# Performance work log

Measured on AMD Instinct MI355X. Metric: run time of the kernel, lower is better.

Reference implementation:

```python
import jax, jax.numpy as jnp
import numpy as np

EPS = 1e-12  # matches torch F.normalize eps

def _l2_normalize(x):
    n = jnp.linalg.norm(x, axis=-1, keepdims=True)
    return x / jnp.maximum(n, EPS)

def setup_inputs() -> dict:
    key = jax.random.key(0)
    k1, k2, k3 = jax.random.split(key, 3)
    B, D, C = 2048, 1024, 65536
    return {
        "query": jax.random.normal(k1, (B, D), dtype=jnp.float32),
        "memory_keys": jax.random.normal(k2, (C, D), dtype=jnp.float32),
        "memory_values": jax.random.normal(k3, (C, D), dtype=jnp.float32),
        "memory_usage": jnp.zeros((C,), dtype=jnp.float32),
        "k": 8,
    }

def reference(query, memory_keys, memory_values, memory_usage, k):
    # cosine similarity: [B, C]
    qn = _l2_normalize(query)
    mn = _l2_normalize(memory_keys)
    sims = jnp.matmul(qn, mn.T)
    # top-k indices per query: [B, k]
    _, indices = jax.lax.top_k(sims, k)
    # gather retrieved keys/values: [B, k, D]
    retrieved_keys = memory_keys[indices]
    retrieved_values = memory_values[indices]
    # usage scatter-add (+1 per retrieved slot), vectorized form of the loop
    capacity = memory_usage.shape[0]
    counts = jax.ops.segment_sum(
        jnp.ones(indices.size, dtype=memory_usage.dtype),
        indices.reshape(-1),
        num_segments=capacity,
    )
    usage_new = memory_usage + counts
    return retrieved_keys, retrieved_values, usage_new
```

## Files before the change

kernel.cpp:

```cpp
#include <hip/hip_runtime.h>
#include <math.h>

#define BQ 2048
#define DD 1024
#define CC 65536
#define KSEL 8
#define NSTRIPE 32
#define SC (CC / NSTRIPE)
#define GTM 128
#define GTN 128
#define GBK 32
#define NTILES (SC / GTN)
#define LCAND 8
#define TRES 32

typedef unsigned int u32;
typedef unsigned short ushort_t;
typedef __attribute__((ext_vector_type(8))) short bf16x8;
typedef __attribute__((ext_vector_type(4))) float f32x4;


#define FENCE() asm volatile("" ::: "memory")
#define LGKM0() asm volatile("s_waitcnt lgkmcnt(0)" ::: "memory")

__device__ __forceinline__ ushort_t f2bf(float f) {
    u32 u = __builtin_bit_cast(u32, f);
    return (ushort_t)((u + 0x7FFFu + ((u >> 16) & 1u)) >> 16);
}

__device__ __forceinline__ void gl_lds16(const ushort_t* g, ushort_t* l) {
    __builtin_amdgcn_global_load_lds(
        (const __attribute__((address_space(1))) u32*)g,
        (__attribute__((address_space(3))) u32*)l, 16, 0, 0);
}

__global__ __launch_bounds__(256) void normconv_kernel(
    const float* __restrict__ q, const float* __restrict__ keys,
    double* __restrict__ qinv, double* __restrict__ kinv,
    ushort_t* __restrict__ qn, ushort_t* __restrict__ kn)
{
    __shared__ double red[4];
    const int row = blockIdx.x;
    const int t = threadIdx.x;
    const bool iskey = row < CC;
    const float* src = iskey ? keys + (size_t)row * DD
                             : q + (size_t)(row - CC) * DD;
    float4 v = ((const float4*)src)[t];
    double s = (double)v.x * v.x + (double)v.y * v.y +
               (double)v.z * v.z + (double)v.w * v.w;
    for (int off = 32; off > 0; off >>= 1) s += __shfl_down(s, off);
    if ((t & 63) == 0) red[t >> 6] = s;
    __syncthreads();
    const double tot = red[0] + red[1] + red[2] + red[3];
    const double inv = 1.0 / fmax(sqrt(tot), 1e-12);
    if (t == 0) {
        if (iskey) kinv[row] = inv; else qinv[row - CC] = inv;
    }
    const float invf = (float)inv;
    ushort4 o;
    o.x = f2bf(v.x * invf); o.y = f2bf(v.y * invf);
    o.z = f2bf(v.z * invf); o.w = f2bf(v.w * invf);
    ushort_t* dst = iskey ? kn + (size_t)row * DD
                          : qn + (size_t)(row - CC) * DD;
    ((ushort4*)dst)[t] = o;
}

__global__ __launch_bounds__(256, 2) void gemm_topk_kernel(
    const ushort_t* __restrict__ qn, const ushort_t* __restrict__ kn,
    unsigned* __restrict__ cand)
{
    __shared__ ushort_t As[2][GTM * GBK];
    __shared__ ushort_t Bs[2][GTN * GBK];
    __shared__ float tilebuf[GTM][65];

    const int tid = threadIdx.x;
    const int wid = tid >> 6;
    const int lane = tid & 63;
    const int wy = wid >> 1, wx = wid & 1;
    const int l15 = lane & 15, quad = lane >> 4;

    const int flat = blockIdx.y * 16 + blockIdx.x;
    const int swz  = (flat & 7) * 64 + (flat >> 3);
    const int bx = swz & 15, by = swz >> 4;
    const int m0 = bx * GTM;
    const int sbase = by * SC;

    const int e0 = tid, e1 = tid + 256;
    const int ks0 = (((e0 & 3) ^ ((e0 >> 3) & 3)) * 8);
    const int ks1 = (((e1 & 3) ^ ((e1 >> 3) & 3)) * 8);
    const ushort_t* gA0 = qn + (size_t)(m0 + (e0 >> 2)) * DD + ks0;
    const ushort_t* gA1 = qn + (size_t)(m0 + (e1 >> 2)) * DD + ks1;
    const ushort_t* gB0 = kn + (size_t)(sbase + (e0 >> 2)) * DD + ks0;
    const ushort_t* gB1 = kn + (size_t)(sbase + (e1 >> 2)) * DD + ks1;

#define STAGE(buf, k0_) do {                         \
        gl_lds16(gA0 + (k0_), As[buf] + e0 * 8);     \
        gl_lds16(gA1 + (k0_), As[buf] + e1 * 8);     \
        gl_lds16(gB0 + (k0_), Bs[buf] + e0 * 8);     \
        gl_lds16(gB1 + (k0_), Bs[buf] + e1 * 8);     \
    } while (0)

    float tv[LCAND];
    int ti[LCAND];
#pragma unroll
    for (int l = 0; l < LCAND; ++l) { tv[l] = -3.0e38f; ti[l] = 0; }
    float minv = -3.0e38f;
    int minpos = 0;

    const int swz15 = (l15 >> 1) & 3;

    STAGE(0, 0);

    for (int nt = 0; nt < NTILES; ++nt) {
        const int cbase = sbase + nt * GTN;

        f32x4 acc[4][4];
#pragma unroll
        for (int i = 0; i < 4; ++i)
#pragma unroll
            for (int j = 0; j < 4; ++j) acc[i][j] = (f32x4)0.0f;

#pragma unroll 2
        for (int kt = 0; kt < DD / GBK; ++kt) {
            const int cur = kt & 1;
            if (kt < DD / GBK - 1) {
                STAGE(cur ^ 1, (kt + 1) * GBK);
                asm volatile("s_waitcnt vmcnt(4)" ::: "memory");
            } else if (nt < NTILES - 1) {
                gB0 += (size_t)GTN * DD;
                gB1 += (size_t)GTN * DD;
                STAGE(cur ^ 1, 0);
                asm volatile("s_waitcnt vmcnt(4)" ::: "memory");
            } else {
                asm volatile("s_waitcnt vmcnt(0)" ::: "memory");
            }
            __builtin_amdgcn_s_barrier();
            FENCE();
            __builtin_amdgcn_s_setprio(1);

            bf16x8 af[4], bfr[4];
#pragma unroll
            for (int ri = 0; ri < 4; ++ri)
                af[ri] = *(const bf16x8*)(As[cur] +
                    (wy * 64 + ri * 16 + l15) * GBK + ((quad ^ swz15) * 8));
#pragma unroll
            for (int ci = 0; ci < 4; ++ci)
                bfr[ci] = *(const bf16x8*)(Bs[cur] +
                    (wx * 64 + ci * 16 + l15) * GBK + ((quad ^ swz15) * 8));
#pragma unroll
            for (int ri = 0; ri < 4; ++ri)
#pragma unroll
                for (int ci = 0; ci < 4; ++ci)
                    acc[ri][ci] = __builtin_amdgcn_mfma_f32_16x16x32_bf16(
                        af[ri], bfr[ci], acc[ri][ci], 0, 0, 0);

            __builtin_amdgcn_s_setprio(0);
            FENCE();
            __builtin_amdgcn_s_barrier();
            FENCE();
        }

        for (int cc2 = 0; cc2 < 2; ++cc2) {
            LGKM0();
            __builtin_amdgcn_s_barrier();
            FENCE();
            if (wx == cc2) {
#pragma unroll
                for (int ri = 0; ri < 4; ++ri)
#pragma unroll
                    for (int ci = 0; ci < 4; ++ci)
#pragma unroll
                        for (int r = 0; r < 4; ++r)
                            tilebuf[wy * 64 + ri * 16 + quad * 4 + r][ci * 16 + l15] =
                                acc[ri][ci][r];
            }
            LGKM0();
            __builtin_amdgcn_s_barrier();
            FENCE();
            {
                const int rr = tid & 127;
                const int jb = (tid >> 7) << 5;
                const int gc0 = cbase + cc2 * 64 + jb;
                for (int j = 0; j < 32; ++j) {
                    float v = tilebuf[rr][jb + j];
                    if (v > minv) {
                        tv[minpos] = v; ti[minpos] = gc0 + j;
                        minv = tv[0]; minpos = 0;
#pragma unroll
                        for (int l = 1; l < LCAND; ++l)
                            if (tv[l] < minv) { minv = tv[l]; minpos = l; }
                    }
                }
            }
        }
    }

    LGKM0();
    __builtin_amdgcn_s_barrier();
    FENCE();
    if (tid >= 128) {
        const int r2 = tid - 128;
#pragma unroll
        for (int l = 0; l < LCAND; ++l) {
            tilebuf[r2][l] = tv[l];
            tilebuf[r2][16 + l] = __int_as_float(ti[l]);
        }
    }
    LGKM0();
    __builtin_amdgcn_s_barrier();
    FENCE();
    if (tid < GTM) {
#pragma unroll
        for (int c = 0; c < LCAND; ++c) {
            float v = tilebuf[tid][c];
            int idx = __float_as_int(tilebuf[tid][16 + c]);
            if (v > minv) {
                tv[minpos] = v; ti[minpos] = idx;
                minv = tv[0]; minpos = 0;
#pragma unroll
                for (int l = 1; l < LCAND; ++l)
                    if (tv[l] < minv) { minv = tv[l]; minpos = l; }
            }
        }
        unsigned* dst = cand + (size_t)(m0 + tid) * (NSTRIPE * LCAND) + by * LCAND;
#pragma unroll
        for (int l = 0; l < LCAND; ++l)
            dst[l] = ((unsigned)f2bf(tv[l]) << 16) | (unsigned)(ti[l] & 0xFFFF);
    }
#undef STAGE
}

__global__ __launch_bounds__(256) void merge_kernel(
    const int* __restrict__ cand, int* __restrict__ sel_idx,
    float* __restrict__ counts)
{
    const int gid = blockIdx.x * 256 + threadIdx.x;
    if (gid < CC) counts[gid] = 0.0f;
    const int row = gid >> 6;
    const int lane = threadIdx.x & 63;
    const int* cv = cand + (size_t)row * (NSTRIPE * LCAND);
    int v[4];
#pragma unroll
    for (int u = 0; u < 4; ++u) v[u] = cv[lane + 64 * u];
    for (int r = 0; r < TRES; ++r) {
        int bv = v[0];
#pragma unroll
        for (int u = 1; u < 4; ++u) bv = max(bv, v[u]);
#pragma unroll
        for (int off = 1; off < 64; off <<= 1) bv = max(bv, __shfl_xor(bv, off));
#pragma unroll
        for (int u = 0; u < 4; ++u)
            if (v[u] == bv) v[u] = (int)0x80000000;
        if (lane == 0) sel_idx[row * TRES + r] = bv & 0xFFFF;
    }
}

__global__ __launch_bounds__(256) void rescore_kernel(
    const float* __restrict__ q, const float* __restrict__ keys,
    const double* __restrict__ qinv, const double* __restrict__ kinv,
    const int* __restrict__ sel_idx, double* __restrict__ sel_val)
{
    const int pair = (blockIdx.x * 256 + threadIdx.x) >> 6;
    const int lane = threadIdx.x & 63;
    const int b = pair >> 5;
    const int c = sel_idx[pair];
    const float4* qr = (const float4*)(q + (size_t)b * DD);
    const float4* kr = (const float4*)(keys + (size_t)c * DD);
    double s = 0.0;
#pragma unroll
    for (int u = 0; u < 4; ++u) {
        float4 a = qr[lane + 64 * u];
        float4 k4 = kr[lane + 64 * u];
        s += (double)a.x * k4.x + (double)a.y * k4.y +
             (double)a.z * k4.z + (double)a.w * k4.w;
    }
    for (int off = 32; off > 0; off >>= 1) s += __shfl_down(s, off);
    if (lane == 0) sel_val[pair] = s * qinv[b] * kinv[c];
}

__global__ __launch_bounds__(256) void finalize_kernel(
    const double* __restrict__ sel_val, const int* __restrict__ sel_idx,
    int* __restrict__ topk_idx, float* __restrict__ counts)
{
    const int b = blockIdx.x * 256 + threadIdx.x;
    if (b >= BQ) return;
    double bv[KSEL]; int bi[KSEL];
#pragma unroll
    for (int j = 0; j < KSEL; ++j) { bv[j] = -1.0e300; bi[j] = 0x7fffffff; }
    for (int t = 0; t < TRES; ++t) {
        double v = sel_val[b * TRES + t];
        int idx = sel_idx[b * TRES + t];
        int p = KSEL;
        while (p > 0 && (v > bv[p - 1] || (v == bv[p - 1] && idx < bi[p - 1]))) --p;
        if (p < KSEL) {
            for (int s = KSEL - 1; s > p; --s) { bv[s] = bv[s - 1]; bi[s] = bi[s - 1]; }
            bv[p] = v; bi[p] = idx;
        }
    }
    for (int j = 0; j < KSEL; ++j) {
        topk_idx[b * KSEL + j] = bi[j];
        atomicAdd(&counts[bi[j]], 1.0f);
    }
}

__global__ __launch_bounds__(256) void gather_kernel(
    const float* __restrict__ keys, const float* __restrict__ values,
    const int* __restrict__ topk_idx, float* __restrict__ out_k,
    float* __restrict__ out_v)
{
    const int pair = blockIdx.x;
    const int c = topk_idx[pair];
    const int t = threadIdx.x;
    const float4* ks = (const float4*)(keys + (size_t)c * DD);
    const float4* vs = (const float4*)(values + (size_t)c * DD);
    float4* ok = (float4*)out_k + (size_t)pair * (DD / 4);
    float4* ov = (float4*)out_v + (size_t)pair * (DD / 4);
    ok[t] = ks[t];
    ov[t] = vs[t];
}

__global__ __launch_bounds__(256) void usage_kernel(
    const float* __restrict__ usage_in, const float* __restrict__ counts,
    float* __restrict__ out_u)
{
    const int c = blockIdx.x * 256 + threadIdx.x;
    out_u[c] = usage_in[c] + counts[c];
}

extern "C" void kernel_launch(void* const* d_in, const int* in_sizes, int n_in,
                              void* d_out, int out_size, void* d_ws, size_t ws_size,
                              hipStream_t stream)
{
    const float* q      = (const float*)d_in[0];
    const float* keys   = (const float*)d_in[1];
    const float* values = (const float*)d_in[2];
    const float* usage  = (const float*)d_in[3];

    char* ws = (char*)d_ws;
    double* qinv     = (double*)(ws + 0);
    double* kinv     = (double*)(ws + 16384);
    ushort_t* qn     = (ushort_t*)(ws + 540672);
    float* counts    = (float*)(ws + 540672);
    int* sel_idx     = (int*)(ws + 802816);
    double* sel_val  = (double*)(ws + 1064960);
    int* topk        = (int*)(ws + 1589248);
    unsigned* cand   = (unsigned*)(ws + 4734976);

    float* out_k = (float*)d_out;
    float* out_v = out_k + (size_t)BQ * KSEL * DD;
    float* out_u = out_v + (size_t)BQ * KSEL * DD;
    ushort_t* kn = (ushort_t*)d_out;

    normconv_kernel<<<CC + BQ, 256, 0, stream>>>(q, keys, qinv, kinv, qn, kn);

    dim3 g2(BQ / GTM, NSTRIPE);
    gemm_topk_kernel<<<g2, 256, 0, stream>>>(qn, kn, cand);

    merge_kernel<<<BQ / 4, 256, 0, stream>>>((const int*)cand, sel_idx, counts);

    rescore_kernel<<<(BQ * TRES) / 4, 256, 0, stream>>>(q, keys, qinv, kinv,
                                                        sel_idx, sel_val);

    finalize_kernel<<<BQ / 256, 256, 0, stream>>>(sel_val, sel_idx, topk, counts);

    gather_kernel<<<BQ * KSEL, 256, 0, stream>>>(keys, values, topk, out_k, out_v);

    usage_kernel<<<CC / 256, 256, 0, stream>>>(usage, counts, out_u);
}
```

Before: 1.129 ms.

## Shrink GEMM epilogue tile buffer for higher occupancy; restructure rescore per query

The GEMM+top-k kernel now writes its accumulator tile to shared memory in four 32-column chunks instead of two 64-column chunks. This halves the tilebuf footprint and lets launch bounds request 3 blocks per CU instead of 2, at the cost of more barriers per tile. The rescore kernel now uses one block per query, staging the query row in shared memory and looping its 4 waves over the 32 candidates. This avoids reloading the query row from global memory for every candidate.

```diff
diff --git a/kernel.cpp b/kernel.cpp
--- a/kernel.cpp
+++ b/kernel.cpp
@@ -65,13 +65,13 @@
     ((ushort4*)dst)[t] = o;
 }
 
-__global__ __launch_bounds__(256, 2) void gemm_topk_kernel(
+__global__ __launch_bounds__(256, 3) void gemm_topk_kernel(
     const ushort_t* __restrict__ qn, const ushort_t* __restrict__ kn,
     unsigned* __restrict__ cand)
 {
     __shared__ ushort_t As[2][GTM * GBK];
     __shared__ ushort_t Bs[2][GTN * GBK];
-    __shared__ float tilebuf[GTM][65];
+    __shared__ float tilebuf[GTM][33];
 
     const int tid = threadIdx.x;
     const int wid = tid >> 6;
@@ -160,28 +160,29 @@
             FENCE();
         }
 
-        for (int cc2 = 0; cc2 < 2; ++cc2) {
+        for (int c4 = 0; c4 < 4; ++c4) {
             LGKM0();
             __builtin_amdgcn_s_barrier();
             FENCE();
-            if (wx == cc2) {
+            if (wx == (c4 >> 1)) {
+                const int cilo = (c4 & 1) * 2;
 #pragma unroll
                 for (int ri = 0; ri < 4; ++ri)
 #pragma unroll
-                    for (int ci = 0; ci < 4; ++ci)
+                    for (int cx = 0; cx < 2; ++cx)
 #pragma unroll
                         for (int r = 0; r < 4; ++r)
-                            tilebuf[wy * 64 + ri * 16 + quad * 4 + r][ci * 16 + l15] =
-                                acc[ri][ci][r];
+                            tilebuf[wy * 64 + ri * 16 + quad * 4 + r][cx * 16 + l15] =
+                                acc[ri][cilo + cx][r];
             }
             LGKM0();
             __builtin_amdgcn_s_barrier();
             FENCE();
             {
                 const int rr = tid & 127;
-                const int jb = (tid >> 7) << 5;
-                const int gc0 = cbase + cc2 * 64 + jb;
-                for (int j = 0; j < 32; ++j) {
+                const int jb = (tid >> 7) << 4;
+                const int gc0 = cbase + c4 * 32 + jb;
+                for (int j = 0; j < 16; ++j) {
                     float v = tilebuf[rr][jb + j];
                     if (v > minv) {
                         tv[minpos] = v; ti[minpos] = gc0 + j;
@@ -260,22 +261,27 @@
     const double* __restrict__ qinv, const double* __restrict__ kinv,
     const int* __restrict__ sel_idx, double* __restrict__ sel_val)
 {
-    const int pair = (blockIdx.x * 256 + threadIdx.x) >> 6;
-    const int lane = threadIdx.x & 63;
-    const int b = pair >> 5;
-    const int c = sel_idx[pair];
-    const float4* qr = (const float4*)(q + (size_t)b * DD);
-    const float4* kr = (const float4*)(keys + (size_t)c * DD);
-    double s = 0.0;
-#pragma unroll
-    for (int u = 0; u < 4; ++u) {
-        float4 a = qr[lane + 64 * u];
-        float4 k4 = kr[lane + 64 * u];
-        s += (double)a.x * k4.x + (double)a.y * k4.y +
-             (double)a.z * k4.z + (double)a.w * k4.w;
-    }
-    for (int off = 32; off > 0; off >>= 1) s += __shfl_down(s, off);
-    if (lane == 0) sel_val[pair] = s * qinv[b] * kinv[c];
+    __shared__ float qs[DD];
+    const int b = blockIdx.x;
+    const int t = threadIdx.x;
+    ((float4*)qs)[t] = ((const float4*)(q + (size_t)b * DD))[t];
+    __syncthreads();
+    const int wv = t >> 6, lane = t & 63;
+    const double qi = qinv[b];
+    for (int cc = wv; cc < TRES; cc += 4) {
+        const int c = sel_idx[b * TRES + cc];
+        const float4* kr = (const float4*)(keys + (size_t)c * DD);
+        double s = 0.0;
+#pragma unroll
+        for (int u = 0; u < 4; ++u) {
+            float4 a = ((const float4*)qs)[lane + 64 * u];
+            float4 k4 = kr[lane + 64 * u];
+            s += (double)a.x * k4.x + (double)a.y * k4.y +
+                 (double)a.z * k4.z + (double)a.w * k4.w;
+        }
+        for (int off = 32; off > 0; off >>= 1) s += __shfl_down(s, off);
+        if (lane == 0) sel_val[b * TRES + cc] = s * qi * kinv[c];
+    }
 }
 
 __global__ __launch_bounds__(256) void finalize_kernel(
@@ -358,8 +364,7 @@
 
     merge_kernel<<<BQ / 4, 256, 0, stream>>>((const int*)cand, sel_idx, counts);
 
-    rescore_kernel<<<(BQ * TRES) / 4, 256, 0, stream>>>(q, keys, qinv, kinv,
-                                                        sel_idx, sel_val);
+    rescore_kernel<<<BQ, 256, 0, stream>>>(q, keys, qinv, kinv, sel_idx, sel_val);
 
     finalize_kernel<<<BQ / 256, 256, 0, stream>>>(sel_val, sel_idx, topk, counts);
 
```

After: 1.133 ms. About the same (+0.4%).
